# Performance work log

Measured on AMD Instinct MI355X. Metric: run time of the kernel, lower is better.

The kernel has to match this reference:

```python
import jax, jax.numpy as jnp
import numpy as np

NUM_SEGMENTS = 128  # num_total_segments


def setup_inputs() -> dict:
    key = jax.random.key(0)
    k1, k2 = jax.random.split(key)
    B, C, Hp, Wp = 2, 768, 28, 28
    Hi, Wi = 392, 392
    F_semantic_patches = jax.random.normal(k1, (B, C, Hp, Wp), dtype=jnp.float32)
    segmentation_mask = jax.random.randint(k2, (B, Hi, Wi), 0, NUM_SEGMENTS, dtype=jnp.int64)
    return {"F_semantic_patches": F_semantic_patches, "segmentation_mask": segmentation_mask}


def reference(F_semantic_patches, segmentation_mask):
    S = NUM_SEGMENTS
    B, C, Hp, Wp = F_semantic_patches.shape
    _, Hi, Wi = segmentation_mask.shape

    # F.interpolate(mode='nearest') to (Hp, Wp): src index = floor(dst * in/out)
    ih = (jnp.arange(Hp) * Hi) // Hp  # [Hp]
    iw = (jnp.arange(Wp) * Wi) // Wp  # [Wp]
    seg_feat = segmentation_mask[:, ih[:, None], iw[None, :]]  # [B,Hp,Wp] int

    # flatten features to [B*Hp*Wp, C] (permute 0,2,3,1 then reshape)
    flat_feat = jnp.transpose(F_semantic_patches, (0, 2, 3, 1)).reshape(-1, C)
    batch_idx = jnp.arange(B, dtype=seg_feat.dtype)[:, None, None]
    gid = (batch_idx * S + jnp.clip(seg_feat, 0, S - 1)).reshape(-1)  # [B*Hp*Wp]

    # scatter_mean over global segment ids, dim_size = B*S
    sums = jax.ops.segment_sum(flat_feat, gid, num_segments=B * S)  # [B*S, C]
    counts = jax.ops.segment_sum(jnp.ones_like(gid, dtype=flat_feat.dtype), gid,
                                 num_segments=B * S)  # [B*S]
    cnt = counts[:, None]
    # mean with nan_to_num(nan=0.0): empty segments -> 0
    seg_avg = jnp.where(cnt > 0, sums / jnp.maximum(cnt, 1), jnp.zeros_like(sums))

    # gather back at full pixel resolution
    pid = (batch_idx * S + jnp.clip(segmentation_mask, 0, S - 1)).reshape(-1)  # [B*Hi*Wi]
    painted = seg_avg[pid].reshape(B, Hi, Wi, C)  # [B,Hi,Wi,C]
    return jnp.transpose(painted, (0, 3, 1, 2))  # [B,C,Hi,Wi]
```

## Files before the change

### kernel.cpp

```cpp
#include <hip/hip_runtime.h>

#define NSEG 128
#define BB 2
#define CC 768
#define HP 28
#define WP 28
#define HI 392
#define WI 392
#define NPIX (HI*WI)
#define NPIX4 (NPIX/4)
#define CH_PER_BLK 128

__global__ void pid_kernel(const int* __restrict__ mask, unsigned int* __restrict__ sb) {
    int g = blockIdx.x * blockDim.x + threadIdx.x;
    if (g >= BB * NPIX4) return;
    int4 m = ((const int4*)mask)[g];
    unsigned int s0 = (unsigned int)min(max(m.x, 0), NSEG - 1);
    unsigned int s1 = (unsigned int)min(max(m.y, 0), NSEG - 1);
    unsigned int s2 = (unsigned int)min(max(m.z, 0), NSEG - 1);
    unsigned int s3 = (unsigned int)min(max(m.w, 0), NSEG - 1);
    sb[g] = s0 | (s1 << 8) | (s2 << 16) | (s3 << 24);
}

__global__ void accum_kernel(const float* __restrict__ F, const int* __restrict__ mask,
                             float* __restrict__ sums, float* __restrict__ counts) {
    int cell = blockIdx.x;
    int b = cell / (HP * WP);
    int rem = cell - b * (HP * WP);
    int hp = rem / WP;
    int wp = rem - hp * WP;
    int m = mask[(size_t)b * NPIX + (hp * 14) * WI + (wp * 14)];
    int s = min(max(m, 0), NSEG - 1);
    for (int c = threadIdx.x; c < CC; c += blockDim.x) {
        float v = F[((b * CC + c) * HP + hp) * WP + wp];
        atomicAdd(&sums[(size_t)(b * CC + c) * NSEG + s], v);
    }
    if (threadIdx.x == 0) atomicAdd(&counts[b * NSEG + s], 1.0f);
}

__global__ void div_kernel(float* __restrict__ sums, const float* __restrict__ counts) {
    int i = blockIdx.x * blockDim.x + threadIdx.x;
    int b = i / (CC * NSEG);
    int s = i & (NSEG - 1);
    float cnt = counts[b * NSEG + s];
    float v = sums[i];
    sums[i] = (cnt > 0.0f) ? (v / cnt) : 0.0f;
}

__global__ __launch_bounds__(256) void paint_kernel(const float* __restrict__ avg,
                                                    const unsigned int* __restrict__ sb,
                                                    float* __restrict__ out) {
    int b = blockIdx.z;
    int g = blockIdx.x * blockDim.x + threadIdx.x;
    if (g >= NPIX4) return;
    unsigned int packed = sb[(size_t)b * NPIX4 + g];
    int s0 = packed & 255;
    int s1 = (packed >> 8) & 255;
    int s2 = (packed >> 16) & 255;
    int s3 = (packed >> 24) & 255;
    int c0 = blockIdx.y * CH_PER_BLK;
    const float* tbl = avg + (size_t)(b * CC + c0) * NSEG;
    float4* outp = (float4*)out + (size_t)(b * CC + c0) * NPIX4 + g;
    #pragma unroll 4
    for (int i = 0; i < CH_PER_BLK; ++i) {
        const float* t = tbl + (size_t)i * NSEG;
        float4 v = make_float4(t[s0], t[s1], t[s2], t[s3]);
        outp[(size_t)i * NPIX4] = v;
    }
}

extern "C" void kernel_launch(void* const* d_in, const int* in_sizes, int n_in,
                              void* d_out, int out_size, void* d_ws, size_t ws_size,
                              hipStream_t stream) {
    const float* F = (const float*)d_in[0];
    const int* mask = (const int*)d_in[1];
    float* out = (float*)d_out;

    float* sums = (float*)d_ws;
    float* counts = sums + BB * CC * NSEG;
    unsigned int* sb = (unsigned int*)(counts + BB * NSEG);

    hipMemsetAsync(d_ws, 0, (size_t)(BB * CC * NSEG + BB * NSEG) * sizeof(float), stream);

    int ngroups = BB * NPIX4;
    pid_kernel<<<(ngroups + 255) / 256, 256, 0, stream>>>(mask, sb);
    accum_kernel<<<BB * HP * WP, 256, 0, stream>>>(F, mask, sums, counts);
    div_kernel<<<(BB * CC * NSEG) / 256, 256, 0, stream>>>(sums, counts);
    paint_kernel<<<dim3((NPIX4 + 255) / 256, CC / CH_PER_BLK, BB), 256, 0, stream>>>(sums, sb, out);
}
```

Measured before the change: 1.199 ms.

## Interleave channel pairs in segment table and use nontemporal stores in paint

The divide kernel now rewrites the per-channel segment averages so that each pair of channels is interleaved as float2 entries. The paint kernel can then fetch two channels per gather and write two float4 rows per iteration. Output stores use nontemporal hints to avoid polluting cache with the large write stream. The channel-per-block count is also changed. This cuts the number of gather loads per output, at the cost of an in-place interleave that relies on a block-wide sync.

Result: faster. 988.9 us (-17.5%).

```diff
diff --git a/kernel.cpp b/kernel.cpp
--- a/kernel.cpp
+++ b/kernel.cpp
@@ -3,13 +3,16 @@
 #define NSEG 128
 #define BB 2
 #define CC 768
+#define CC2 (CC/2)
 #define HP 28
 #define WP 28
 #define HI 392
 #define WI 392
 #define NPIX (HI*WI)
 #define NPIX4 (NPIX/4)
-#define CH_PER_BLK 128
+#define CPB2 32
+
+typedef float f32x4 __attribute__((ext_vector_type(4)));
 
 __global__ void pid_kernel(const int* __restrict__ mask, unsigned int* __restrict__ sb) {
     int g = blockIdx.x * blockDim.x + threadIdx.x;
@@ -38,16 +41,21 @@
     if (threadIdx.x == 0) atomicAdd(&counts[b * NSEG + s], 1.0f);
 }
 
-__global__ void div_kernel(float* __restrict__ sums, const float* __restrict__ counts) {
-    int i = blockIdx.x * blockDim.x + threadIdx.x;
-    int b = i / (CC * NSEG);
-    int s = i & (NSEG - 1);
+__global__ __launch_bounds__(128) void div_kernel(float* __restrict__ sums,
+                                                  const float* __restrict__ counts) {
+    int pair = blockIdx.x;
+    int b = pair / CC2;
+    int s = threadIdx.x;
+    float* base = sums + ((size_t)pair << 8);
     float cnt = counts[b * NSEG + s];
-    float v = sums[i];
-    sums[i] = (cnt > 0.0f) ? (v / cnt) : 0.0f;
+    float v0 = base[s];
+    float v1 = base[s + NSEG];
+    float inv = (cnt > 0.0f) ? (1.0f / cnt) : 0.0f;
+    __syncthreads();
+    ((float2*)base)[s] = make_float2(v0 * inv, v1 * inv);
 }
 
-__global__ __launch_bounds__(256) void paint_kernel(const float* __restrict__ avg,
+__global__ __launch_bounds__(256) void paint_kernel(const float2* __restrict__ avg2,
                                                     const unsigned int* __restrict__ sb,
                                                     float* __restrict__ out) {
     int b = blockIdx.z;
@@ -58,14 +66,17 @@
     int s1 = (packed >> 8) & 255;
     int s2 = (packed >> 16) & 255;
     int s3 = (packed >> 24) & 255;
-    int c0 = blockIdx.y * CH_PER_BLK;
-    const float* tbl = avg + (size_t)(b * CC + c0) * NSEG;
-    float4* outp = (float4*)out + (size_t)(b * CC + c0) * NPIX4 + g;
-    #pragma unroll 4
-    for (int i = 0; i < CH_PER_BLK; ++i) {
-        const float* t = tbl + (size_t)i * NSEG;
-        float4 v = make_float4(t[s0], t[s1], t[s2], t[s3]);
-        outp[(size_t)i * NPIX4] = v;
+    int p2 = blockIdx.y * CPB2;
+    const float2* tbl = avg2 + ((size_t)(b * CC2 + p2) << 7);
+    f32x4* outp = (f32x4*)out + (size_t)(b * CC + 2 * p2) * NPIX4 + g;
+    #pragma unroll 8
+    for (int i = 0; i < CPB2; ++i) {
+        const float2* t = tbl + ((size_t)i << 7);
+        float2 a = t[s0], bb = t[s1], c = t[s2], d = t[s3];
+        f32x4 lo = {a.x, bb.x, c.x, d.x};
+        f32x4 hi = {a.y, bb.y, c.y, d.y};
+        __builtin_nontemporal_store(lo, outp + (size_t)(2 * i) * NPIX4);
+        __builtin_nontemporal_store(hi, outp + (size_t)(2 * i + 1) * NPIX4);
     }
 }
 
@@ -80,11 +91,12 @@
     float* counts = sums + BB * CC * NSEG;
     unsigned int* sb = (unsigned int*)(counts + BB * NSEG);
 
-    hipMemsetAsync(d_ws, 0, (size_t)(BB * CC * NSEG + BB * NSEG) * sizeof(float), stream);
+    (void)hipMemsetAsync(d_ws, 0, (size_t)(BB * CC * NSEG + BB * NSEG) * sizeof(float), stream);
 
     int ngroups = BB * NPIX4;
     pid_kernel<<<(ngroups + 255) / 256, 256, 0, stream>>>(mask, sb);
     accum_kernel<<<BB * HP * WP, 256, 0, stream>>>(F, mask, sums, counts);
-    div_kernel<<<(BB * CC * NSEG) / 256, 256, 0, stream>>>(sums, counts);
-    paint_kernel<<<dim3((NPIX4 + 255) / 256, CC / CH_PER_BLK, BB), 256, 0, stream>>>(sums, sb, out);
+    div_kernel<<<BB * CC2, 128, 0, stream>>>(sums, counts);
+    paint_kernel<<<dim3((NPIX4 + 255) / 256, CC2 / CPB2, BB), 256, 0, stream>>>(
+        (const float2*)sums, sb, out);
 }
```

## Restructure paint kernel: per-channel LDS table, pixel-span loop, nontemporal stores

Applied to the files above, without the earlier changes.

The paint kernel now gives each block one (batch, channel) pair and a quarter of the pixel range. It loads that channel's 128-entry segment-average table into shared memory and loops over packed segment ids, so table lookups come from LDS instead of global/L1 gathers. Output writes use nontemporal stores to avoid polluting the cache. The trade-off is that the packed segment-id buffer is re-read once per channel (768x per batch) rather than once per 128 channels, though it is small and likely stays cached.

Result: faster. 1.006 ms (-16.1%).

```diff
diff --git a/kernel.cpp b/kernel.cpp
--- a/kernel.cpp
+++ b/kernel.cpp
@@ -9,7 +9,10 @@
 #define WI 392
 #define NPIX (HI*WI)
 #define NPIX4 (NPIX/4)
-#define CH_PER_BLK 128
+#define NSPLIT 4
+#define SPAN (NPIX4/NSPLIT)
+
+typedef float f32x4 __attribute__((ext_vector_type(4)));
 
 __global__ void pid_kernel(const int* __restrict__ mask, unsigned int* __restrict__ sb) {
     int g = blockIdx.x * blockDim.x + threadIdx.x;
@@ -50,22 +53,22 @@
 __global__ __launch_bounds__(256) void paint_kernel(const float* __restrict__ avg,
                                                     const unsigned int* __restrict__ sb,
                                                     float* __restrict__ out) {
+    __shared__ float tbl[NSEG];
+    int c = blockIdx.y;
     int b = blockIdx.z;
-    int g = blockIdx.x * blockDim.x + threadIdx.x;
-    if (g >= NPIX4) return;
-    unsigned int packed = sb[(size_t)b * NPIX4 + g];
-    int s0 = packed & 255;
-    int s1 = (packed >> 8) & 255;
-    int s2 = (packed >> 16) & 255;
-    int s3 = (packed >> 24) & 255;
-    int c0 = blockIdx.y * CH_PER_BLK;
-    const float* tbl = avg + (size_t)(b * CC + c0) * NSEG;
-    float4* outp = (float4*)out + (size_t)(b * CC + c0) * NPIX4 + g;
+    if (threadIdx.x < NSEG)
+        tbl[threadIdx.x] = avg[(((size_t)(b * CC + c)) << 7) + threadIdx.x];
+    __syncthreads();
+
+    const unsigned int* sbp = sb + (size_t)b * NPIX4;
+    f32x4* outp = (f32x4*)out + (size_t)(b * CC + c) * NPIX4;
+    int gend = (blockIdx.x + 1) * SPAN;
     #pragma unroll 4
-    for (int i = 0; i < CH_PER_BLK; ++i) {
-        const float* t = tbl + (size_t)i * NSEG;
-        float4 v = make_float4(t[s0], t[s1], t[s2], t[s3]);
-        outp[(size_t)i * NPIX4] = v;
+    for (int g = blockIdx.x * SPAN + threadIdx.x; g < gend; g += 256) {
+        unsigned int p = sbp[g];
+        f32x4 v = {tbl[p & 255], tbl[(p >> 8) & 255],
+                   tbl[(p >> 16) & 255], tbl[(p >> 24) & 255]};
+        __builtin_nontemporal_store(v, outp + g);
     }
 }
 
@@ -80,11 +83,11 @@
     float* counts = sums + BB * CC * NSEG;
     unsigned int* sb = (unsigned int*)(counts + BB * NSEG);
 
-    hipMemsetAsync(d_ws, 0, (size_t)(BB * CC * NSEG + BB * NSEG) * sizeof(float), stream);
+    (void)hipMemsetAsync(d_ws, 0, (size_t)(BB * CC * NSEG + BB * NSEG) * sizeof(float), stream);
 
     int ngroups = BB * NPIX4;
     pid_kernel<<<(ngroups + 255) / 256, 256, 0, stream>>>(mask, sb);
     accum_kernel<<<BB * HP * WP, 256, 0, stream>>>(F, mask, sums, counts);
     div_kernel<<<(BB * CC * NSEG) / 256, 256, 0, stream>>>(sums, counts);
-    paint_kernel<<<dim3((NPIX4 + 255) / 256, CC / CH_PER_BLK, BB), 256, 0, stream>>>(sums, sb, out);
+    paint_kernel<<<dim3(NSPLIT, CC, BB), 256, 0, stream>>>(sums, sb, out);
 }
```
